# Optimization experiments

Hardware: AMD Instinct MI355X
Metric: run time of the kernel (lower is better)

Reference implementation:

```python
import jax, jax.numpy as jnp
import numpy as np

D_MODEL, N_HEAD, D_HEAD = 1024, 16, 64
QLEN, MLEN, BSZ = 1024, 512, 4
KLEN = QLEN + MLEN
RLEN = QLEN + KLEN
SCALE = 1.0 / (D_HEAD ** 0.5)
LN_EPS = 1e-12


def rel_shift(x, klen):
    # x: [i, j, b, n] -> shifted [i, klen, b, n]
    i, j, b, n = x.shape
    x = x.reshape(j, i, b, n)[1:].reshape(i, j - 1, b, n)
    return x[:, :klen]


def layer_norm(x, gamma, beta, eps=LN_EPS):
    mu = jnp.mean(x, axis=-1, keepdims=True)
    var = jnp.mean(jnp.square(x - mu), axis=-1, keepdims=True)
    return (x - mu) * jax.lax.rsqrt(var + eps) * gamma + beta


def setup_inputs() -> dict:
    key = jax.random.key(0)
    ks = jax.random.split(key, 16)
    std = 0.02
    h = jax.random.normal(ks[0], (QLEN, BSZ, D_MODEL), jnp.float32)
    r = jax.random.normal(ks[1], (RLEN, BSZ, D_MODEL), jnp.float32)
    mems = jax.random.normal(ks[2], (MLEN, BSZ, D_MODEL), jnp.float32)
    # binary float mask (1 = masked), broadcast over head dim
    attn_mask = (jax.random.uniform(ks[3], (QLEN, KLEN, BSZ, 1)) < 0.1).astype(jnp.float32)
    # one-hot segment matrix over 2 segment classes
    seg_ids = jax.random.randint(ks[4], (QLEN, KLEN, BSZ), 0, 2)
    seg_mat = jax.nn.one_hot(seg_ids, 2, dtype=jnp.float32)
    Wq = std * jax.random.normal(ks[5], (D_MODEL, N_HEAD, D_HEAD), jnp.float32)
    Wk = std * jax.random.normal(ks[6], (D_MODEL, N_HEAD, D_HEAD), jnp.float32)
    Wv = std * jax.random.normal(ks[7], (D_MODEL, N_HEAD, D_HEAD), jnp.float32)
    Wo = std * jax.random.normal(ks[8], (D_MODEL, N_HEAD, D_HEAD), jnp.float32)
    Wr = std * jax.random.normal(ks[9], (D_MODEL, N_HEAD, D_HEAD), jnp.float32)
    r_w_bias = jnp.zeros((N_HEAD, D_HEAD), jnp.float32)
    r_r_bias = jnp.zeros((N_HEAD, D_HEAD), jnp.float32)
    r_s_bias = jnp.zeros((N_HEAD, D_HEAD), jnp.float32)
    seg_embed = std * jax.random.normal(ks[10], (2, N_HEAD, D_HEAD), jnp.float32)
    ln_gamma = jnp.ones((D_MODEL,), jnp.float32)
    ln_beta = jnp.zeros((D_MODEL,), jnp.float32)
    return dict(h=h, r=r, mems=mems, attn_mask=attn_mask, seg_mat=seg_mat,
                Wq=Wq, Wk=Wk, Wv=Wv, Wo=Wo, Wr=Wr,
                r_w_bias=r_w_bias, r_r_bias=r_r_bias, r_s_bias=r_s_bias,
                seg_embed=seg_embed, ln_gamma=ln_gamma, ln_beta=ln_beta)


def reference(h, r, mems, attn_mask, seg_mat, Wq, Wk, Wv, Wo, Wr,
              r_w_bias, r_r_bias, r_s_bias, seg_embed, ln_gamma, ln_beta):
    cat = jnp.concatenate([mems, h], axis=0)  # [klen, b, d_model]
    q_head = jnp.einsum('ibh,hnd->ibnd', h, Wq)
    k_head_h = jnp.einsum('jbh,hnd->jbnd', cat, Wk)
    v_head_h = jnp.einsum('jbh,hnd->jbnd', cat, Wv)
    k_head_r = jnp.einsum('jbh,hnd->jbnd', r, Wr)

    klen = k_head_h.shape[0]
    ac = jnp.einsum('ibnd,jbnd->ijbn', q_head + r_w_bias, k_head_h)
    bd = jnp.einsum('ibnd,jbnd->ijbn', q_head + r_r_bias, k_head_r)
    bd = rel_shift(bd, klen)
    ef = jnp.einsum('ibnd,snd->ibns', q_head + r_s_bias, seg_embed)
    ef = jnp.einsum('ijbs,ibns->ijbn', seg_mat, ef)

    attn_score = (ac + bd + ef) * SCALE - 1e30 * attn_mask
    attn_prob = jax.nn.softmax(attn_score, axis=1)
    attn_vec = jnp.einsum('ijbn,jbnd->ibnd', attn_prob, v_head_h)

    attn_out = jnp.einsum('ibnd,hnd->ibh', attn_vec, Wo) + h  # residual
    return layer_norm(attn_out, ln_gamma, ln_beta)
```

## Files before the change

### kernel.cpp

```cpp
#include <hip/hip_runtime.h>

typedef unsigned short u16;
typedef __attribute__((ext_vector_type(8))) short bf16x8;
typedef __attribute__((ext_vector_type(4))) float f32x4;

constexpr int DM = 1024;
constexpr int NH = 16;
constexpr int DH = 64;
constexpr int QL = 1024;
constexpr int ML = 512;
constexpr int KL = 1536;
constexpr int RL = 2560;
constexpr int BS = 4;
constexpr int JT = KL / 64;
constexpr float SCALE = 0.125f;

static __device__ __forceinline__ u16 f2bf(float f) {
    unsigned u = __float_as_uint(f);
    u += 0x7fffu + ((u >> 16) & 1u);
    return (u16)(u >> 16);
}

static __device__ __forceinline__ void glds16(const u16* g, u16* l) {
    __builtin_amdgcn_global_load_lds(
        (const __attribute__((address_space(1))) unsigned int*)g,
        (__attribute__((address_space(3))) unsigned int*)l,
        16, 0, 0);
}

__global__ __launch_bounds__(256) void prep_kernel(
    const float* __restrict__ mems, const float* __restrict__ h,
    const float* __restrict__ r, const float* __restrict__ Wo,
    const float* __restrict__ mask, const float* __restrict__ segm,
    const float* __restrict__ Wq, const float* __restrict__ Wk,
    const float* __restrict__ Wv, const float* __restrict__ Wr,
    u16* __restrict__ catb, u16* __restrict__ rb, u16* __restrict__ wob,
    u16* __restrict__ WqT, u16* __restrict__ WkT,
    u16* __restrict__ WvT, u16* __restrict__ WrT,
    ulonglong2* __restrict__ pk)
{
    __shared__ float smem[64 * 65];
    const int id = blockIdx.x;
    const int t = threadIdx.x;

    if (id < 17408) {
        const long C0 = (long)ML * BS * DM;
        const long C1 = (long)KL * BS * DM;
        const long C2 = C1 + (long)RL * BS * DM;
        long g = ((long)id * 256 + t) * 4;
        const float* src; u16* dst;
        if (g < C0)      { src = mems + g;        dst = catb + g; }
        else if (g < C1) { src = h + (g - C0);    dst = catb + g; }
        else if (g < C2) { src = r + (g - C1);    dst = rb + (g - C1); }
        else             { src = Wo + (g - C2);   dst = wob + (g - C2); }
        float4 v = *(const float4*)src;
        unsigned lo = (unsigned)f2bf(v.x) | ((unsigned)f2bf(v.y) << 16);
        unsigned hi = (unsigned)f2bf(v.z) | ((unsigned)f2bf(v.w) << 16);
        *(uint2*)dst = make_uint2(lo, hi);
        return;
    }
    if (id < 18432) {
        float (*tile)[65] = (float(*)[65])smem;
        const int local = id - 17408;
        const float* W; u16* WT;
        switch (local >> 8) {
            case 0:  W = Wq; WT = WqT; break;
            case 1:  W = Wk; WT = WkT; break;
            case 2:  W = Wv; WT = WvT; break;
            default: W = Wr; WT = WrT; break;
        }
        const int k0 = (local & 15) * 64, n0 = ((local >> 4) & 15) * 64;
        const int tr = t >> 6, tc = t & 63;
        #pragma unroll
        for (int rr = 0; rr < 16; rr++) {
            int rw = tr + rr * 4;
            tile[rw][tc] = W[(size_t)(k0 + rw) * DM + n0 + tc];
        }
        __syncthreads();
        #pragma unroll
        for (int rr = 0; rr < 16; rr++) {
            int n = tr + rr * 4;
            WT[(size_t)(n0 + n) * DM + k0 + tc] = f2bf(tile[tc][n]);
        }
        return;
    }
    {
        float* mk = smem;
        float* sg = smem + 256;
        const int local = id - 18432;
        const int i = local / JT, jt = local - i * JT;
        const size_t base = ((size_t)i * KL + jt * 64) * BS;
        mk[t] = mask[base + t];
        float2 s2 = ((const float2*)(segm + base * 2))[t];
        sg[t] = s2.y;
        __syncthreads();
        const int b = t >> 6, lane = t & 63;
        const unsigned long long mb = __ballot(mk[lane * 4 + b] > 0.5f);
        const unsigned long long sb = __ballot(sg[lane * 4 + b] > 0.5f);
        if (lane == 0) {
            ulonglong2 v; v.x = mb; v.y = sb;
            pk[((size_t)b * QL + i) * JT + jt] = v;
        }
    }
}

__global__ __launch_bounds__(256) void proj_kernel(
    const u16* __restrict__ hb, const u16* __restrict__ catb,
    const u16* __restrict__ rb,
    const u16* __restrict__ WqT, const u16* __restrict__ WkT,
    const u16* __restrict__ WvT, const u16* __restrict__ WrT,
    float* __restrict__ q_s, u16* __restrict__ k_s,
    u16* __restrict__ v_s, u16* __restrict__ kr_s)
{
    __shared__ u16 a_lds[128][32];
    __shared__ u16 b_lds[128][32];
    const int id = blockIdx.x;
    const u16 *A, *B; void* C; int SEQ, MODE, local;
    if (id < 256)       { A = hb;   B = WqT; C = q_s;  SEQ = QL; MODE = 1; local = id; }
    else if (id < 640)  { A = catb; B = WkT; C = k_s;  SEQ = KL; MODE = 2; local = id - 256; }
    else if (id < 1024) { A = catb; B = WvT; C = v_s;  SEQ = KL; MODE = 2; local = id - 640; }
    else                { A = rb;   B = WrT; C = kr_s; SEQ = RL; MODE = 2; local = id - 1024; }
    const int bm = local >> 3, bnn = local & 7;

    const int t = threadIdx.x;
    const int w = t >> 6, lane = t & 63, l15 = lane & 15, q4 = lane >> 4;
    const int wm = (w >> 1) * 64, wn = (w & 1) * 64;
    const int srow = w * 32 + (lane >> 2);
    const int scol = (lane & 3) * 8;
    const u16* Ab = A + (size_t)(bm * 128 + srow) * DM + scol;
    const u16* Bb = B + (size_t)(bnn * 128 + srow) * DM + scol;
    u16* a_dst = &a_lds[w * 32][0];
    u16* b_dst = &b_lds[w * 32][0];

    f32x4 acc[4][4] = {};

    for (int k0 = 0; k0 < DM; k0 += 32) {
        __syncthreads();
        glds16(Ab + k0,           a_dst);
        glds16(Ab + k0 + 16 * DM, a_dst + 16 * 32);
        glds16(Bb + k0,           b_dst);
        glds16(Bb + k0 + 16 * DM, b_dst + 16 * 32);
        __syncthreads();
        bf16x8 af[4], bf[4];
        #pragma unroll
        for (int rt = 0; rt < 4; rt++)
            af[rt] = *(const bf16x8*)&a_lds[wm + rt * 16 + l15][q4 * 8];
        #pragma unroll
        for (int ct = 0; ct < 4; ct++)
            bf[ct] = *(const bf16x8*)&b_lds[wn + ct * 16 + l15][q4 * 8];
        #pragma unroll
        for (int rt = 0; rt < 4; rt++)
            #pragma unroll
            for (int ct = 0; ct < 4; ct++)
                acc[rt][ct] = __builtin_amdgcn_mfma_f32_16x16x32_bf16(
                    af[rt], bf[ct], acc[rt][ct], 0, 0, 0);
    }

    #pragma unroll
    for (int rt = 0; rt < 4; rt++)
      #pragma unroll
      for (int ct = 0; ct < 4; ct++)
        #pragma unroll
        for (int rg = 0; rg < 4; rg++) {
            const int R = bm * 128 + wm + rt * 16 + q4 * 4 + rg;
            const int Cc = bnn * 128 + wn + ct * 16 + l15;
            const float v = acc[rt][ct][rg];
            const int sq = R >> 2, bb = R & 3, hn = Cc >> 6, dd = Cc & 63;
            const size_t idx = ((size_t)(bb * NH + hn) * SEQ + sq) * DH + dd;
            if (MODE == 1) ((float*)C)[idx] = v;
            else           ((u16*)C)[idx]  = f2bf(v);
        }
}

__global__ __launch_bounds__(256) void vtrans_kernel(
    const u16* __restrict__ v_s, u16* __restrict__ vt_s)
{
    __shared__ u16 tl[64][72];
    const int j0 = blockIdx.x * 64;
    const int bn = blockIdx.y;
    const u16* vin = v_s + (size_t)bn * KL * DH;
    u16* vout = vt_s + (size_t)bn * DH * KL;
    const int t = threadIdx.x;
    const int r = t >> 3, c8 = (t & 7) * 8;
    #pragma unroll
    for (int it = 0; it < 64; it += 32)
        *(uint4*)&tl[r + it][c8] = *(const uint4*)(vin + (size_t)(j0 + r + it) * DH + c8);
    __syncthreads();
    #pragma unroll
    for (int it = 0; it < 64; it += 32) {
        const int d = r + it;
        u16 tmp[8];
        #pragma unroll
        for (int jj = 0; jj < 8; jj++) tmp[jj] = tl[c8 + jj][d];
        *(uint4*)&vout[(size_t)d * KL + j0 + c8] = *(const uint4*)tmp;
    }
}

__global__ __launch_bounds__(256) void ogemm_kernel(
    const u16* __restrict__ A, const u16* __restrict__ B,
    float* __restrict__ Cout)
{
    __shared__ u16 a_lds[128][32];
    __shared__ u16 b_lds[128][32];
    const int bm = blockIdx.x, bnn = blockIdx.y;
    const int t = threadIdx.x;
    const int w = t >> 6, lane = t & 63, l15 = lane & 15, q4 = lane >> 4;
    const int wm = (w >> 1) * 64, wn = (w & 1) * 64;
    const int srow = w * 32 + (lane >> 2);
    const int scol = (lane & 3) * 8;
    const u16* Ab = A + (size_t)(bm * 128 + srow) * DM + scol;
    const u16* Bb = B + (size_t)(bnn * 128 + srow) * DM + scol;
    u16* a_dst = &a_lds[w * 32][0];
    u16* b_dst = &b_lds[w * 32][0];

    f32x4 acc[4][4] = {};

    for (int k0 = 0; k0 < DM; k0 += 32) {
        __syncthreads();
        glds16(Ab + k0,           a_dst);
        glds16(Ab + k0 + 16 * DM, a_dst + 16 * 32);
        glds16(Bb + k0,           b_dst);
        glds16(Bb + k0 + 16 * DM, b_dst + 16 * 32);
        __syncthreads();
        bf16x8 af[4], bf[4];
        #pragma unroll
        for (int rt = 0; rt < 4; rt++)
            af[rt] = *(const bf16x8*)&a_lds[wm + rt * 16 + l15][q4 * 8];
        #pragma unroll
        for (int ct = 0; ct < 4; ct++)
            bf[ct] = *(const bf16x8*)&b_lds[wn + ct * 16 + l15][q4 * 8];
        #pragma unroll
        for (int rt = 0; rt < 4; rt++)
            #pragma unroll
            for (int ct = 0; ct < 4; ct++)
                acc[rt][ct] = __builtin_amdgcn_mfma_f32_16x16x32_bf16(
                    af[rt], bf[ct], acc[rt][ct], 0, 0, 0);
    }

    #pragma unroll
    for (int rt = 0; rt < 4; rt++)
      #pragma unroll
      for (int ct = 0; ct < 4; ct++)
        #pragma unroll
        for (int rg = 0; rg < 4; rg++) {
            const int R = bm * 128 + wm + rt * 16 + q4 * 4 + rg;
            const int C = bnn * 128 + wn + ct * 16 + l15;
            Cout[(size_t)R * DM + C] = acc[rt][ct][rg];
        }
}

__global__ __launch_bounds__(256, 3) void attn_kernel(
    const float* __restrict__ q_s, const u16* __restrict__ k_s,
    const u16* __restrict__ vt_s, const u16* __restrict__ kr_s,
    const ulonglong2* __restrict__ pk,
    const float* __restrict__ rwb, const float* __restrict__ rrb,
    const float* __restrict__ rsb, const float* __restrict__ seg_embed,
    u16* __restrict__ av_s)
{
    __shared__ u16 k2[2][64][32];
    __shared__ u16 vt2[2][64][32];
    __shared__ u16 krl[128][64];
    __shared__ u16 p_lds[4][16][72];
    __shared__ float e_lds[2][64];

    const int bn = blockIdx.x;
    const int itile = blockIdx.y;
    const int b = bn >> 4, n = bn & 15;
    const int t = threadIdx.x;
    const int w = t >> 6, lane = t & 63, l15 = lane & 15, q4 = lane >> 4;
    const int i0 = itile * 64;
    const int ib = i0 + w * 16;

    const float* q_bn = q_s + (size_t)bn * QL * DH;
    const u16* k_bn   = k_s  + (size_t)bn * KL * DH;
    const u16* vt_bn  = vt_s + (size_t)bn * DH * KL;
    const u16* kr_bn  = kr_s + (size_t)bn * RL * DH;
    const ulonglong2* pk_b = pk + (size_t)b * QL * JT;

    if (t < 128) {
        const int rr = t >> 1, s = t & 1;
        const float* qrow = q_bn + (size_t)(i0 + rr) * DH;
        const float* se = seg_embed + (s * NH + n) * DH;
        const float* bias = rsb + n * DH;
        float acc = 0.f;
        #pragma unroll 16
        for (int d = 0; d < DH; d++) acc += (qrow[d] + bias[d]) * se[d];
        e_lds[s][rr] = acc;
    }

    bf16x8 qw[2], qr[2];
    {
        const float* qrow = q_bn + (size_t)(ib + l15) * DH;
        const float* bw = rwb + n * DH;
        const float* br = rrb + n * DH;
        #pragma unroll
        for (int kk = 0; kk < 2; kk++) {
            const int dbase = kk * 32 + q4 * 8;
            #pragma unroll
            for (int j = 0; j < 8; j++) {
                float qv = qrow[dbase + j];
                qw[kk][j] = (short)f2bf(qv + bw[dbase + j]);
                qr[kk][j] = (short)f2bf(qv + br[dbase + j]);
            }
        }
    }

    const int srow = lane >> 2;
    const int sseg = (lane & 3) * 8;
    const u16* kg = k_bn  + (size_t)(w * 16 + srow) * DH + sseg;
    const u16* vg = vt_bn + (size_t)(w * 16 + srow) * KL + sseg;
    u16* kd0 = &k2[0][w * 16][0];
    u16* kd1 = &k2[1][w * 16][0];
    u16* vd0 = &vt2[0][w * 16][0];
    u16* vd1 = &vt2[1][w * 16][0];

    const int krow = lane >> 3;
    const int ksrcseg = (lane & 7) ^ krow;
    u16* krd = &krl[w * 32][0];

    f32x4 o[4] = {};
    float l_r[4] = {0.f, 0.f, 0.f, 0.f};

    const int lrb = 48 - w * 16 + l15;
    const int sA = ((q4)     ^ (l15 & 7)) * 8;
    const int sB = ((q4 + 4) ^ (l15 & 7)) * 8;

    for (int jt = 0; jt < JT; jt++) {
        const int j0 = jt * 64;
        const int Pbase = j0 + QL - i0 - 63;
        __syncthreads();
        glds16(kg + (size_t)j0 * DH,      kd0);
        glds16(kg + (size_t)j0 * DH + 32, kd1);
        glds16(vg + j0,                   vd0);
        glds16(vg + j0 + 32,              vd1);
        {
            const u16* krg = kr_bn + (size_t)(Pbase + w * 32 + krow) * DH + ksrcseg * 8;
            #pragma unroll
            for (int m = 0; m < 4; m++)
                glds16(krg + (size_t)m * 8 * DH, krd + m * 8 * 64);
        }
        ulonglong2 mp[4];
        #pragma unroll
        for (int rg = 0; rg < 4; rg++)
            mp[rg] = pk_b[(size_t)(ib + q4 * 4 + rg) * JT + jt];
        __syncthreads();

        f32x4 sac[4] = {};
        #pragma unroll
        for (int ct = 0; ct < 4; ct++) {
            bf16x8 kb0 = *(const bf16x8*)&k2[0][ct * 16 + l15][q4 * 8];
            bf16x8 kb1 = *(const bf16x8*)&k2[1][ct * 16 + l15][q4 * 8];
            sac[ct] = __builtin_amdgcn_mfma_f32_16x16x32_bf16(qw[0], kb0, sac[ct], 0, 0, 0);
            sac[ct] = __builtin_amdgcn_mfma_f32_16x16x32_bf16(qw[1], kb1, sac[ct], 0, 0, 0);
        }

        f32x4 bacc[5] = {};
        #pragma unroll
        for (int wc = 0; wc < 5; wc++) {
            bf16x8 b0 = *(const bf16x8*)&krl[lrb + wc * 16][sA];
            bf16x8 b1 = *(const bf16x8*)&krl[lrb + wc * 16][sB];
            bacc[wc] = __builtin_amdgcn_mfma_f32_16x16x32_bf16(qr[0], b0, bacc[wc], 0, 0, 0);
            bacc[wc] = __builtin_amdgcn_mfma_f32_16x16x32_bf16(qr[1], b1, bacc[wc], 0, 0, 0);
        }

        #pragma unroll
        for (int rg = 0; rg < 4; rg++) {
            const int row = q4 * 4 + rg;
            const int v = l15 + 15 - row;
            const int srcl = (q4 << 4) | (v & 15);
            float sh[5];
            #pragma unroll
            for (int w5 = 0; w5 < 5; w5++)
                sh[w5] = __shfl(bacc[w5][rg], srcl, 64);
            const float e0 = e_lds[0][w * 16 + row];
            const float e1 = e_lds[1][w * 16 + row];
            float s0 = 0.f;
            #pragma unroll
            for (int ct = 0; ct < 4; ct++) {
                const float bd = (v < 16) ? sh[ct] : sh[ct + 1];
                const int bit = ct * 16 + l15;
                const float ef = ((mp[rg].y >> bit) & 1ull) ? e1 : e0;
                const float s = (sac[ct][rg] + bd + ef) * SCALE;
                float p = __expf(s);
                p = ((mp[rg].x >> bit) & 1ull) ? 0.f : p;
                p_lds[w][row][ct * 16 + l15] = f2bf(p);
                s0 += p;
            }
            l_r[rg] += s0;
        }

        #pragma unroll
        for (int kk = 0; kk < 2; kk++) {
            bf16x8 pf = *(const bf16x8*)&p_lds[w][l15][kk * 32 + q4 * 8];
            #pragma unroll
            for (int dt = 0; dt < 4; dt++) {
                bf16x8 vf = *(const bf16x8*)&vt2[kk][dt * 16 + l15][q4 * 8];
                o[dt] = __builtin_amdgcn_mfma_f32_16x16x32_bf16(pf, vf, o[dt], 0, 0, 0);
            }
        }
    }

    #pragma unroll
    for (int rg = 0; rg < 4; rg++) {
        #pragma unroll
        for (int off = 1; off < 16; off <<= 1)
            l_r[rg] += __shfl_xor(l_r[rg], off, 64);
        l_r[rg] = 1.f / l_r[rg];
    }
    #pragma unroll
    for (int dt = 0; dt < 4; dt++)
        #pragma unroll
        for (int rg = 0; rg < 4; rg++) {
            const int row = q4 * 4 + rg;
            const int ii = ib + row;
            const int d = dt * 16 + l15;
            const float v = o[dt][rg] * l_r[rg];
            av_s[(size_t)(ii * BS + b) * DM + n * DH + d] = f2bf(v);
        }
}

__global__ __launch_bounds__(256) void ln_kernel(
    const float* __restrict__ ao, const float* __restrict__ h,
    const float* __restrict__ gamma, const float* __restrict__ beta,
    float* __restrict__ out)
{
    __shared__ float red[8];
    const int row = blockIdx.x, t = threadIdx.x;
    const float* a  = ao + (size_t)row * DM;
    const float* hh = h  + (size_t)row * DM;
    float4 av = *(const float4*)(a + t * 4);
    float4 hv = *(const float4*)(hh + t * 4);
    const float x0 = av.x + hv.x, x1 = av.y + hv.y;
    const float x2 = av.z + hv.z, x3 = av.w + hv.w;
    float s = x0 + x1 + x2 + x3;
    float s2 = x0 * x0 + x1 * x1 + x2 * x2 + x3 * x3;
    #pragma unroll
    for (int off = 1; off < 64; off <<= 1) {
        s  += __shfl_xor(s, off, 64);
        s2 += __shfl_xor(s2, off, 64);
    }
    const int w = t >> 6;
    if ((t & 63) == 0) { red[w] = s; red[4 + w] = s2; }
    __syncthreads();
    s  = red[0] + red[1] + red[2] + red[3];
    s2 = red[4] + red[5] + red[6] + red[7];
    const float mu = s * (1.f / DM);
    const float var = s2 * (1.f / DM) - mu * mu;
    const float rstd = rsqrtf(var + 1e-12f);
    float4 g  = *(const float4*)(gamma + t * 4);
    float4 bb = *(const float4*)(beta + t * 4);
    float4 ov;
    ov.x = (x0 - mu) * rstd * g.x + bb.x;
    ov.y = (x1 - mu) * rstd * g.y + bb.y;
    ov.z = (x2 - mu) * rstd * g.z + bb.z;
    ov.w = (x3 - mu) * rstd * g.w + bb.w;
    *(float4*)(out + (size_t)row * DM + t * 4) = ov;
}

extern "C" void kernel_launch(void* const* d_in, const int* in_sizes, int n_in,
                              void* d_out, int out_size, void* d_ws, size_t ws_size,
                              hipStream_t stream) {
    (void)in_sizes; (void)n_in; (void)out_size; (void)ws_size;
    const float* h    = (const float*)d_in[0];
    const float* r    = (const float*)d_in[1];
    const float* mems = (const float*)d_in[2];
    const float* mask = (const float*)d_in[3];
    const float* segm = (const float*)d_in[4];
    const float* Wq   = (const float*)d_in[5];
    const float* Wk   = (const float*)d_in[6];
    const float* Wv   = (const float*)d_in[7];
    const float* Wo   = (const float*)d_in[8];
    const float* Wr   = (const float*)d_in[9];
    const float* rwb  = (const float*)d_in[10];
    const float* rrb  = (const float*)d_in[11];
    const float* rsb  = (const float*)d_in[12];
    const float* semb = (const float*)d_in[13];
    const float* gam  = (const float*)d_in[14];
    const float* bet  = (const float*)d_in[15];
    float* out = (float*)d_out;

    char* wsb = (char*)d_ws;
    size_t off = 0;
    auto alloc = [&](size_t bytes) -> void* {
        void* p = wsb + off; off += (bytes + 255) & ~(size_t)255; return p;
    };
    u16* catb = (u16*)alloc((size_t)KL * BS * DM * 2);
    u16* rb   = (u16*)alloc((size_t)RL * BS * DM * 2);
    u16* WqT  = (u16*)alloc((size_t)DM * DM * 2);
    u16* WkT  = (u16*)alloc((size_t)DM * DM * 2);
    u16* WvT  = (u16*)alloc((size_t)DM * DM * 2);
    u16* WrT  = (u16*)alloc((size_t)DM * DM * 2);
    u16* WoB  = (u16*)alloc((size_t)DM * DM * 2);
    float* q_s = (float*)alloc((size_t)BS * NH * QL * DH * 4);
    u16* k_s  = (u16*)alloc((size_t)BS * NH * KL * DH * 2);
    u16* vt_s = (u16*)alloc((size_t)BS * NH * KL * DH * 2);
    u16* kr_s = (u16*)alloc((size_t)BS * NH * RL * DH * 2 + 8192);
    u16* av_s = (u16*)alloc((size_t)QL * BS * DM * 2);
    float* ao_s = (float*)alloc((size_t)QL * BS * DM * 4);
    ulonglong2* pk = (ulonglong2*)alloc((size_t)BS * QL * JT * 16);
    u16* v_s = (u16*)ao_s;

    prep_kernel<<<43008, 256, 0, stream>>>(mems, h, r, Wo, mask, segm,
                                           Wq, Wk, Wv, Wr,
                                           catb, rb, WoB,
                                           WqT, WkT, WvT, WrT, pk);
    const u16* hb = catb + (size_t)2048 * DM;
    proj_kernel<<<1664, 256, 0, stream>>>(hb, catb, rb, WqT, WkT, WvT, WrT,
                                          q_s, k_s, v_s, kr_s);
    vtrans_kernel<<<dim3(JT, 64), 256, 0, stream>>>(v_s, vt_s);
    attn_kernel<<<dim3(64, 16), 256, 0, stream>>>(q_s, k_s, vt_s, kr_s, pk,
                                                  rwb, rrb, rsb, semb, av_s);
    ogemm_kernel<<<dim3(32, 8), 256, 0, stream>>>(av_s, WoB, ao_s);
    ln_kernel<<<4096, 256, 0, stream>>>(ao_s, h, gam, bet, out);
}
```

Baseline: 516.7 us.

## Double-buffer attention K/V/Kr tiles with async prefetch and swizzled LDS

Restructures the attention loop to double-buffer K, V^T and relative-key tiles in LDS, prefetching tile jt+2 while computing on tile jt with explicit vmcnt waits and raw barriers. It also XOR-swizzles the K/V and P LDS layouts to reduce bank conflicts, which shrinks the P tile padding. Occupancy hint drops from 3 to 2 blocks per CU because LDS use roughly doubles. The aim is to hide global-load latency behind the MFMA and softmax work, at the cost of fewer resident waves and reliance on hand-counted vmcnt values.

```diff
diff --git a/kernel.cpp b/kernel.cpp
--- a/kernel.cpp
+++ b/kernel.cpp
@@ -249,7 +249,100 @@
         }
 }
 
-__global__ __launch_bounds__(256, 3) void attn_kernel(
+#define FBAR() do { asm volatile("" ::: "memory");  \
+                    __builtin_amdgcn_s_barrier();   \
+                    asm volatile("" ::: "memory"); } while (0)
+
+#define STAGE(JT_IDX, KB, VB, KRB, MPC)                                        \
+  {                                                                            \
+    const int j2_ = (JT_IDX) * 64;                                             \
+    const int Pb_ = j2_ + QL - i0 - 63;                                        \
+    glds16(kg + (size_t)j2_ * DH,      &KB[0][w * 16][0]);                     \
+    glds16(kg + (size_t)j2_ * DH + 32, &KB[1][w * 16][0]);                     \
+    glds16(vg + j2_,                   &VB[0][w * 16][0]);                     \
+    glds16(vg + j2_ + 32,              &VB[1][w * 16][0]);                     \
+    const u16* krg_ = kr_bn + (size_t)(Pb_ + w * 32 + krow) * DH + ksrcseg * 8;\
+    _Pragma("unroll")                                                          \
+    for (int m_ = 0; m_ < 4; m_++)                                             \
+      glds16(krg_ + (size_t)m_ * 8 * DH, &KRB[w * 32 + m_ * 8][0]);            \
+    _Pragma("unroll")                                                          \
+    for (int rg_ = 0; rg_ < 4; rg_++)                                          \
+      MPC[rg_] = pk_b[(size_t)(ib + q4 * 4 + rg_) * JT + (JT_IDX)];            \
+  }
+
+#define ATTN_STEP(JT_IDX, KB, VB, KRB, MPC)                                    \
+  {                                                                            \
+    const int jt_ = (JT_IDX);                                                  \
+                                      \
+    f32x4 sac[4] = {};                                                         \
+    _Pragma("unroll")                                                          \
+    for (int ct = 0; ct < 4; ct++) {                                           \
+      bf16x8 kb0 = *(const bf16x8*)&KB[0][ct * 16 + l15][(q4 ^ ksw) * 8];      \
+      bf16x8 kb1 = *(const bf16x8*)&KB[1][ct * 16 + l15][(q4 ^ ksw) * 8];      \
+      sac[ct] = __builtin_amdgcn_mfma_f32_16x16x32_bf16(qw[0], kb0, sac[ct], 0, 0, 0); \
+      sac[ct] = __builtin_amdgcn_mfma_f32_16x16x32_bf16(qw[1], kb1, sac[ct], 0, 0, 0); \
+    }                                                                          \
+                    \
+    f32x4 bacc[5] = {};                                                        \
+    _Pragma("unroll")                                                          \
+    for (int wc = 0; wc < 5; wc++) {                                           \
+      bf16x8 b0 = *(const bf16x8*)&KRB[lrb + wc * 16][sA];                     \
+      bf16x8 b1 = *(const bf16x8*)&KRB[lrb + wc * 16][sB];                     \
+      bacc[wc] = __builtin_amdgcn_mfma_f32_16x16x32_bf16(qr[0], b0, bacc[wc], 0, 0, 0); \
+      bacc[wc] = __builtin_amdgcn_mfma_f32_16x16x32_bf16(qr[1], b1, bacc[wc], 0, 0, 0); \
+    }                                                                          \
+                 \
+    _Pragma("unroll")                                                          \
+    for (int rg = 0; rg < 4; rg++) {                                           \
+      const int row = q4 * 4 + rg;                                             \
+      const int v = l15 + 15 - row;                             \
+      const int srcl = (q4 << 4) | (v & 15);                                   \
+      float sh[5];                                                             \
+      _Pragma("unroll")                                                        \
+      for (int w5 = 0; w5 < 5; w5++)                                           \
+        sh[w5] = __shfl(bacc[w5][rg], srcl, 64);                               \
+      const float e0 = e_lds[0][w * 16 + row];                                 \
+      const float e1 = e_lds[1][w * 16 + row];                                 \
+      float s0 = 0.f;                                                          \
+      _Pragma("unroll")                                                        \
+      for (int ct = 0; ct < 4; ct++) {                                         \
+        const float bd = (v < 16) ? sh[ct] : sh[ct + 1];                       \
+        const int bit = ct * 16 + l15;                                         \
+        const float ef = ((MPC[rg].y >> bit) & 1ull) ? e1 : e0;                \
+        const float s = (sac[ct][rg] + bd + ef) * SCALE;                       \
+        float p = __expf(s);                                                   \
+        p = ((MPC[rg].x >> bit) & 1ull) ? 0.f : p;             \
+        const int pg = (2 * ct + (l15 >> 3)) ^ (row & 7);                      \
+        p_lds[w][row][pg * 8 + (l15 & 7)] = f2bf(p);                           \
+        s0 += p;                                                               \
+      }                                                                        \
+      l_r[rg] += s0;                                                           \
+    }                                                                          \
+                   \
+    _Pragma("unroll")                                                          \
+    for (int kk = 0; kk < 2; kk++) {                                           \
+      const int pgr = ((kk * 4 + q4) ^ (l15 & 7)) * 8;                         \
+      bf16x8 pf = *(const bf16x8*)&p_lds[w][l15][pgr];                         \
+      _Pragma("unroll")                                                        \
+      for (int dt = 0; dt < 4; dt++) {                                         \
+        bf16x8 vf = *(const bf16x8*)&VB[kk][dt * 16 + l15][(q4 ^ ksw) * 8];    \
+        o[dt] = __builtin_amdgcn_mfma_f32_16x16x32_bf16(pf, vf, o[dt], 0, 0, 0); \
+      }                                                                        \
+    }                                                                          \
+                                           \
+    if (jt_ < JT - 1) {                                                        \
+      FBAR();                                 \
+      if (jt_ + 2 < JT) {                                                      \
+        STAGE(jt_ + 2, KB, VB, KRB, MPC);       \
+        asm volatile("s_waitcnt vmcnt(12)" ::: "memory");     \
+      } else {                                                                 \
+        asm volatile("s_waitcnt vmcnt(0)" ::: "memory");                       \
+      }                                                                        \
+      FBAR();                                 \
+    }                                                                          \
+  }
+
+__global__ __launch_bounds__(256, 2) void attn_kernel(
     const float* __restrict__ q_s, const u16* __restrict__ k_s,
     const u16* __restrict__ vt_s, const u16* __restrict__ kr_s,
     const ulonglong2* __restrict__ pk,
@@ -257,10 +350,10 @@
     const float* __restrict__ rsb, const float* __restrict__ seg_embed,
     u16* __restrict__ av_s)
 {
-    __shared__ u16 k2[2][64][32];
-    __shared__ u16 vt2[2][64][32];
-    __shared__ u16 krl[128][64];
-    __shared__ u16 p_lds[4][16][72];
+    __shared__ u16 k2[2][2][64][32];
+    __shared__ u16 vt2[2][2][64][32];
+    __shared__ u16 krl[2][128][64];
+    __shared__ u16 p_lds[4][16][64];
     __shared__ float e_lds[2][64];
 
     const int bn = blockIdx.x;
@@ -306,98 +399,31 @@
     }
 
     const int srow = lane >> 2;
-    const int sseg = (lane & 3) * 8;
-    const u16* kg = k_bn  + (size_t)(w * 16 + srow) * DH + sseg;
-    const u16* vg = vt_bn + (size_t)(w * 16 + srow) * KL + sseg;
-    u16* kd0 = &k2[0][w * 16][0];
-    u16* kd1 = &k2[1][w * 16][0];
-    u16* vd0 = &vt2[0][w * 16][0];
-    u16* vd1 = &vt2[1][w * 16][0];
+    const int ssw  = ((lane & 3) ^ ((srow >> 1) & 3)) * 8;
+    const u16* kg = k_bn  + (size_t)(w * 16 + srow) * DH + ssw;
+    const u16* vg = vt_bn + (size_t)(w * 16 + srow) * KL + ssw;
 
     const int krow = lane >> 3;
     const int ksrcseg = (lane & 7) ^ krow;
-    u16* krd = &krl[w * 32][0];
-
-    f32x4 o[4] = {};
-    float l_r[4] = {0.f, 0.f, 0.f, 0.f};
 
     const int lrb = 48 - w * 16 + l15;
     const int sA = ((q4)     ^ (l15 & 7)) * 8;
     const int sB = ((q4 + 4) ^ (l15 & 7)) * 8;
-
-    for (int jt = 0; jt < JT; jt++) {
-        const int j0 = jt * 64;
-        const int Pbase = j0 + QL - i0 - 63;
-        __syncthreads();
-        glds16(kg + (size_t)j0 * DH,      kd0);
-        glds16(kg + (size_t)j0 * DH + 32, kd1);
-        glds16(vg + j0,                   vd0);
-        glds16(vg + j0 + 32,              vd1);
-        {
-            const u16* krg = kr_bn + (size_t)(Pbase + w * 32 + krow) * DH + ksrcseg * 8;
-            #pragma unroll
-            for (int m = 0; m < 4; m++)
-                glds16(krg + (size_t)m * 8 * DH, krd + m * 8 * 64);
-        }
-        ulonglong2 mp[4];
-        #pragma unroll
-        for (int rg = 0; rg < 4; rg++)
-            mp[rg] = pk_b[(size_t)(ib + q4 * 4 + rg) * JT + jt];
-        __syncthreads();
-
-        f32x4 sac[4] = {};
-        #pragma unroll
-        for (int ct = 0; ct < 4; ct++) {
-            bf16x8 kb0 = *(const bf16x8*)&k2[0][ct * 16 + l15][q4 * 8];
-            bf16x8 kb1 = *(const bf16x8*)&k2[1][ct * 16 + l15][q4 * 8];
-            sac[ct] = __builtin_amdgcn_mfma_f32_16x16x32_bf16(qw[0], kb0, sac[ct], 0, 0, 0);
-            sac[ct] = __builtin_amdgcn_mfma_f32_16x16x32_bf16(qw[1], kb1, sac[ct], 0, 0, 0);
-        }
-
-        f32x4 bacc[5] = {};
-        #pragma unroll
-        for (int wc = 0; wc < 5; wc++) {
-            bf16x8 b0 = *(const bf16x8*)&krl[lrb + wc * 16][sA];
-            bf16x8 b1 = *(const bf16x8*)&krl[lrb + wc * 16][sB];
-            bacc[wc] = __builtin_amdgcn_mfma_f32_16x16x32_bf16(qr[0], b0, bacc[wc], 0, 0, 0);
-            bacc[wc] = __builtin_amdgcn_mfma_f32_16x16x32_bf16(qr[1], b1, bacc[wc], 0, 0, 0);
-        }
-
-        #pragma unroll
-        for (int rg = 0; rg < 4; rg++) {
-            const int row = q4 * 4 + rg;
-            const int v = l15 + 15 - row;
-            const int srcl = (q4 << 4) | (v & 15);
-            float sh[5];
-            #pragma unroll
-            for (int w5 = 0; w5 < 5; w5++)
-                sh[w5] = __shfl(bacc[w5][rg], srcl, 64);
-            const float e0 = e_lds[0][w * 16 + row];
-            const float e1 = e_lds[1][w * 16 + row];
-            float s0 = 0.f;
-            #pragma unroll
-            for (int ct = 0; ct < 4; ct++) {
-                const float bd = (v < 16) ? sh[ct] : sh[ct + 1];
-                const int bit = ct * 16 + l15;
-                const float ef = ((mp[rg].y >> bit) & 1ull) ? e1 : e0;
-                const float s = (sac[ct][rg] + bd + ef) * SCALE;
-                float p = __expf(s);
-                p = ((mp[rg].x >> bit) & 1ull) ? 0.f : p;
-                p_lds[w][row][ct * 16 + l15] = f2bf(p);
-                s0 += p;
-            }
-            l_r[rg] += s0;
-        }
-
-        #pragma unroll
-        for (int kk = 0; kk < 2; kk++) {
-            bf16x8 pf = *(const bf16x8*)&p_lds[w][l15][kk * 32 + q4 * 8];
-            #pragma unroll
-            for (int dt = 0; dt < 4; dt++) {
-                bf16x8 vf = *(const bf16x8*)&vt2[kk][dt * 16 + l15][q4 * 8];
-                o[dt] = __builtin_amdgcn_mfma_f32_16x16x32_bf16(pf, vf, o[dt], 0, 0, 0);
-            }
-        }
+    const int ksw = (l15 >> 1) & 3;
+
+    f32x4 o[4] = {};
+    float l_r[4] = {0.f, 0.f, 0.f, 0.f};
+    ulonglong2 mpA[4], mpB[4];
+
+    STAGE(0, k2[0], vt2[0], krl[0], mpA);
+    STAGE(1, k2[1], vt2[1], krl[1], mpB);
+    asm volatile("s_waitcnt vmcnt(12) lgkmcnt(0)" ::: "memory");
+    FBAR();
+
+    #pragma unroll 1
+    for (int jt0 = 0; jt0 < JT; jt0 += 2) {
+        ATTN_STEP(jt0,     k2[0], vt2[0], krl[0], mpA);
+        ATTN_STEP(jt0 + 1, k2[1], vt2[1], krl[1], mpB);
     }
 
     #pragma unroll
```

New measurement: 499.9 us. 1.03x faster.

## Double-buffer attention K/V/Kr/mask tiles with async LDS prefetch and swizzles

Applied to the files above, without the earlier changes.

Restructures the attention loop into a software pipeline. K, V and mask tiles are double-buffered, and the relative-position Kr tile sits in a 4-slot ring so each 64-row slab is loaded once and reused across iterations. Global loads for the next tiles are issued while the current tile computes, with explicit vmcnt waits and raw barriers. Other changes: the mask words are re-laid out per i-tile and staged through LDS, the scale is folded into q so exp2 can be used, masking is done by a large negative score, LDS reads use XOR swizzles to avoid bank conflicts, and MFMA sections run at raised priority. The larger LDS footprint lowers the occupancy hint from 3 to 2 blocks per CU.

```diff
diff --git a/kernel.cpp b/kernel.cpp
--- a/kernel.cpp
+++ b/kernel.cpp
@@ -14,6 +14,7 @@
 constexpr int BS = 4;
 constexpr int JT = KL / 64;
 constexpr float SCALE = 0.125f;
+constexpr float SC2 = 0.125f * 1.4426950408889634f;
 
 static __device__ __forceinline__ u16 f2bf(float f) {
     unsigned u = __float_as_uint(f);
@@ -99,7 +100,7 @@
         const unsigned long long sb = __ballot(sg[lane * 4 + b] > 0.5f);
         if (lane == 0) {
             ulonglong2 v; v.x = mb; v.y = sb;
-            pk[((size_t)b * QL + i) * JT + jt] = v;
+            pk[(((size_t)b * 16 + (i >> 6)) * JT + jt) * 64 + (i & 63)] = v;
         }
     }
 }
@@ -249,7 +250,34 @@
         }
 }
 
-__global__ __launch_bounds__(256, 3) void attn_kernel(
+#define FBAR() do { asm volatile("" ::: "memory");  \
+                    __builtin_amdgcn_s_barrier();   \
+                    asm volatile("" ::: "memory"); } while (0)
+
+#define STAGE_K(TI)                                                            \
+  {                                                                            \
+    glds16(kg + (size_t)(TI) * 64 * DH,      &k2[(TI) & 1][0][w * 16][0]);     \
+    glds16(kg + (size_t)(TI) * 64 * DH + 32, &k2[(TI) & 1][1][w * 16][0]);     \
+  }
+
+#define STAGE_V(TI)                                                            \
+  {                                                                            \
+    glds16(vg + (TI) * 64,      &v2[(TI) & 1][0][w * 16][0]);                  \
+    glds16(vg + (TI) * 64 + 32, &v2[(TI) & 1][1][w * 16][0]);                  \
+  }
+
+#define STAGE_PK(TI)                                                           \
+    glds16((const u16*)(pk_b + ((size_t)(TI) * 64 + lane)),                    \
+           (u16*)&pk_lds[(TI) & 1][0]);
+
+#define STAGE_KR(P)                                                            \
+  {                                                                            \
+    const int br_ = QL - i0 - 63 + (P) * 64 + w * 16 + krow;                   \
+    glds16(kr_bn + (size_t)br_ * DH + ksrcseg * 8,       &krp[(P) & 3][w * 16][0]);     \
+    glds16(kr_bn + (size_t)(br_ + 8) * DH + ksrcseg * 8, &krp[(P) & 3][w * 16 + 8][0]); \
+  }
+
+__global__ __launch_bounds__(256, 2) void attn_kernel(
     const float* __restrict__ q_s, const u16* __restrict__ k_s,
     const u16* __restrict__ vt_s, const u16* __restrict__ kr_s,
     const ulonglong2* __restrict__ pk,
@@ -257,10 +285,11 @@
     const float* __restrict__ rsb, const float* __restrict__ seg_embed,
     u16* __restrict__ av_s)
 {
-    __shared__ u16 k2[2][64][32];
-    __shared__ u16 vt2[2][64][32];
-    __shared__ u16 krl[128][64];
-    __shared__ u16 p_lds[4][16][72];
+    __shared__ u16 k2[2][2][64][32];
+    __shared__ u16 v2[2][2][64][32];
+    __shared__ u16 krp[4][64][64];
+    __shared__ u16 p_lds[4][16][64];
+    __shared__ ulonglong2 pk_lds[2][64];
     __shared__ float e_lds[2][64];
 
     const int bn = blockIdx.x;
@@ -275,7 +304,7 @@
     const u16* k_bn   = k_s  + (size_t)bn * KL * DH;
     const u16* vt_bn  = vt_s + (size_t)bn * DH * KL;
     const u16* kr_bn  = kr_s + (size_t)bn * RL * DH;
-    const ulonglong2* pk_b = pk + (size_t)b * QL * JT;
+    const ulonglong2* pk_b = pk + ((size_t)b * 16 + itile) * JT * 64;
 
     if (t < 128) {
         const int rr = t >> 1, s = t & 1;
@@ -285,7 +314,7 @@
         float acc = 0.f;
         #pragma unroll 16
         for (int d = 0; d < DH; d++) acc += (qrow[d] + bias[d]) * se[d];
-        e_lds[s][rr] = acc;
+        e_lds[s][rr] = acc * SC2;
     }
 
     bf16x8 qw[2], qr[2];
@@ -299,57 +328,52 @@
             #pragma unroll
             for (int j = 0; j < 8; j++) {
                 float qv = qrow[dbase + j];
-                qw[kk][j] = (short)f2bf(qv + bw[dbase + j]);
-                qr[kk][j] = (short)f2bf(qv + br[dbase + j]);
+                qw[kk][j] = (short)f2bf((qv + bw[dbase + j]) * SC2);
+                qr[kk][j] = (short)f2bf((qv + br[dbase + j]) * SC2);
             }
         }
     }
 
     const int srow = lane >> 2;
-    const int sseg = (lane & 3) * 8;
-    const u16* kg = k_bn  + (size_t)(w * 16 + srow) * DH + sseg;
-    const u16* vg = vt_bn + (size_t)(w * 16 + srow) * KL + sseg;
-    u16* kd0 = &k2[0][w * 16][0];
-    u16* kd1 = &k2[1][w * 16][0];
-    u16* vd0 = &vt2[0][w * 16][0];
-    u16* vd1 = &vt2[1][w * 16][0];
+    const int ssw  = ((lane & 3) ^ ((srow >> 1) & 3)) * 8;
+    const u16* kg = k_bn  + (size_t)(w * 16 + srow) * DH + ssw;
+    const u16* vg = vt_bn + (size_t)(w * 16 + srow) * KL + ssw;
 
     const int krow = lane >> 3;
     const int ksrcseg = (lane & 7) ^ krow;
-    u16* krd = &krl[w * 32][0];
+
+    const int sA = ((q4)     ^ (l15 & 7)) * 8;
+    const int sB = ((q4 + 4) ^ (l15 & 7)) * 8;
+    const int ksw = (l15 >> 1) & 3;
+    const int lrb_p = 48 - w * 16;
 
     f32x4 o[4] = {};
     float l_r[4] = {0.f, 0.f, 0.f, 0.f};
 
-    const int lrb = 48 - w * 16 + l15;
-    const int sA = ((q4)     ^ (l15 & 7)) * 8;
-    const int sB = ((q4 + 4) ^ (l15 & 7)) * 8;
-
+    STAGE_K(0); STAGE_V(0); STAGE_PK(0);
+    STAGE_KR(0); STAGE_KR(1);
+    STAGE_K(1); STAGE_V(1); STAGE_PK(1);
+    STAGE_KR(2);
+    asm volatile("s_waitcnt vmcnt(7) lgkmcnt(0)" ::: "memory");
+    FBAR();
+
+    float e_rg[2][4];
+    #pragma unroll
+    for (int rg = 0; rg < 4; rg++) {
+        e_rg[0][rg] = e_lds[0][w * 16 + q4 * 4 + rg];
+        e_rg[1][rg] = e_lds[1][w * 16 + q4 * 4 + rg];
+    }
+
+    #pragma unroll 1
     for (int jt = 0; jt < JT; jt++) {
-        const int j0 = jt * 64;
-        const int Pbase = j0 + QL - i0 - 63;
-        __syncthreads();
-        glds16(kg + (size_t)j0 * DH,      kd0);
-        glds16(kg + (size_t)j0 * DH + 32, kd1);
-        glds16(vg + j0,                   vd0);
-        glds16(vg + j0 + 32,              vd1);
-        {
-            const u16* krg = kr_bn + (size_t)(Pbase + w * 32 + krow) * DH + ksrcseg * 8;
-            #pragma unroll
-            for (int m = 0; m < 4; m++)
-                glds16(krg + (size_t)m * 8 * DH, krd + m * 8 * 64);
-        }
-        ulonglong2 mp[4];
-        #pragma unroll
-        for (int rg = 0; rg < 4; rg++)
-            mp[rg] = pk_b[(size_t)(ib + q4 * 4 + rg) * JT + jt];
-        __syncthreads();
-
+        const int cb = jt & 1;
+
+        __builtin_amdgcn_s_setprio(1);
         f32x4 sac[4] = {};
         #pragma unroll
         for (int ct = 0; ct < 4; ct++) {
-            bf16x8 kb0 = *(const bf16x8*)&k2[0][ct * 16 + l15][q4 * 8];
-            bf16x8 kb1 = *(const bf16x8*)&k2[1][ct * 16 + l15][q4 * 8];
+            bf16x8 kb0 = *(const bf16x8*)&k2[cb][0][ct * 16 + l15][(q4 ^ ksw) * 8];
+            bf16x8 kb1 = *(const bf16x8*)&k2[cb][1][ct * 16 + l15][(q4 ^ ksw) * 8];
             sac[ct] = __builtin_amdgcn_mfma_f32_16x16x32_bf16(qw[0], kb0, sac[ct], 0, 0, 0);
             sac[ct] = __builtin_amdgcn_mfma_f32_16x16x32_bf16(qw[1], kb1, sac[ct], 0, 0, 0);
         }
@@ -357,46 +381,69 @@
         f32x4 bacc[5] = {};
         #pragma unroll
         for (int wc = 0; wc < 5; wc++) {
-            bf16x8 b0 = *(const bf16x8*)&krl[lrb + wc * 16][sA];
-            bf16x8 b1 = *(const bf16x8*)&krl[lrb + wc * 16][sB];
+            const int S = lrb_p + wc * 16;
+            const u16* pr_ = &krp[(jt + (S >> 6)) & 3][(S & 63) + l15][0];
+            bf16x8 b0 = *(const bf16x8*)(pr_ + sA);
+            bf16x8 b1 = *(const bf16x8*)(pr_ + sB);
             bacc[wc] = __builtin_amdgcn_mfma_f32_16x16x32_bf16(qr[0], b0, bacc[wc], 0, 0, 0);
             bacc[wc] = __builtin_amdgcn_mfma_f32_16x16x32_bf16(qr[1], b1, bacc[wc], 0, 0, 0);
         }
+        __builtin_amdgcn_s_setprio(0);
 
         #pragma unroll
         for (int rg = 0; rg < 4; rg++) {
             const int row = q4 * 4 + rg;
+            const ulonglong2 mp = pk_lds[cb][w * 16 + row];
+            const unsigned long long mx = mp.x >> l15;
+            const unsigned long long sy = mp.y >> l15;
             const int v = l15 + 15 - row;
             const int srcl = (q4 << 4) | (v & 15);
             float sh[5];
             #pragma unroll
             for (int w5 = 0; w5 < 5; w5++)
                 sh[w5] = __shfl(bacc[w5][rg], srcl, 64);
-            const float e0 = e_lds[0][w * 16 + row];
-            const float e1 = e_lds[1][w * 16 + row];
+            const float e0 = e_rg[0][rg];
+            const float e1 = e_rg[1][rg];
             float s0 = 0.f;
             #pragma unroll
             for (int ct = 0; ct < 4; ct++) {
                 const float bd = (v < 16) ? sh[ct] : sh[ct + 1];
-                const int bit = ct * 16 + l15;
-                const float ef = ((mp[rg].y >> bit) & 1ull) ? e1 : e0;
-                const float s = (sac[ct][rg] + bd + ef) * SCALE;
-                float p = __expf(s);
-                p = ((mp[rg].x >> bit) & 1ull) ? 0.f : p;
-                p_lds[w][row][ct * 16 + l15] = f2bf(p);
+                const float ef = ((sy >> (ct * 16)) & 1ull) ? e1 : e0;
+                float sarg = sac[ct][rg] + bd + ef;
+                sarg = ((mx >> (ct * 16)) & 1ull) ? -1.0e30f : sarg;
+                const float p = __builtin_amdgcn_exp2f(sarg);
+                const int pg = (2 * ct + (l15 >> 3)) ^ (row & 7);
+                p_lds[w][row][pg * 8 + (l15 & 7)] = f2bf(p);
                 s0 += p;
             }
             l_r[rg] += s0;
         }
 
+        __builtin_amdgcn_s_setprio(1);
         #pragma unroll
         for (int kk = 0; kk < 2; kk++) {
-            bf16x8 pf = *(const bf16x8*)&p_lds[w][l15][kk * 32 + q4 * 8];
+            const int pgr = ((kk * 4 + q4) ^ (l15 & 7)) * 8;
+            bf16x8 pf = *(const bf16x8*)&p_lds[w][l15][pgr];
             #pragma unroll
             for (int dt = 0; dt < 4; dt++) {
-                bf16x8 vf = *(const bf16x8*)&vt2[kk][dt * 16 + l15][q4 * 8];
+                bf16x8 vf = *(const bf16x8*)&v2[cb][kk][dt * 16 + l15][(q4 ^ ksw) * 8];
                 o[dt] = __builtin_amdgcn_mfma_f32_16x16x32_bf16(pf, vf, o[dt], 0, 0, 0);
             }
+        }
+        __builtin_amdgcn_s_setprio(0);
+
+        if (jt < JT - 1) {
+            FBAR();
+            if (jt + 2 < JT) {
+                STAGE_K(jt + 2);
+                STAGE_V(jt + 2);
+                STAGE_PK(jt + 2);
+                STAGE_KR(jt + 3);
+                asm volatile("s_waitcnt vmcnt(7)" ::: "memory");
+            } else {
+                asm volatile("s_waitcnt vmcnt(0)" ::: "memory");
+            }
+            FBAR();
         }
     }
 
```

After: 514.8 us. About the same (-0.4%).
